# Kernel tuning notes

Hardware: AMD Instinct MI355X
Metric: run time of the kernel (lower is better)

Reference implementation:

```python
import jax, jax.numpy as jnp
import numpy as np
import math

B, S, D, H = 2, 2048, 1024, 16
DK = D // H


def setup_inputs() -> dict:
    key = jax.random.key(0)
    ks = jax.random.split(key, 10)
    sc = 1.0 / math.sqrt(D)
    inp = {
        "Q_input": jax.random.normal(ks[0], (B, S, D), dtype=jnp.float32),
        "Wq_w": jax.random.normal(ks[1], (D, D), dtype=jnp.float32) * sc,
        "Wq_b": jnp.zeros((D,), dtype=jnp.float32),
        "Wk_w": jax.random.normal(ks[2], (D, D), dtype=jnp.float32) * sc,
        "Wk_b": jnp.zeros((D,), dtype=jnp.float32),
        "Wv_w": jax.random.normal(ks[3], (D, D), dtype=jnp.float32) * sc,
        "Wv_b": jnp.zeros((D,), dtype=jnp.float32),
        "Wo_w": jax.random.normal(ks[4], (D, D), dtype=jnp.float32) * sc,
        "Wo_b": jnp.zeros((D,), dtype=jnp.float32),
        # causal mask, broadcast over batch and heads: [1,1,S,S]
        "mask": jnp.tril(jnp.ones((S, S), dtype=jnp.int32))[None, None],
    }
    return inp


def reference(Q_input, Wq_w, Wq_b, Wk_w, Wk_b, Wv_w, Wv_b, Wo_w, Wo_b, mask):
    b, s, _ = Q_input.shape
    # linear projections (torch Linear: x @ W^T + b)
    Q = Q_input @ Wq_w.T + Wq_b
    K = Q_input @ Wk_w.T + Wk_b
    V = Q_input @ Wv_w.T + Wv_b
    # [b, h, s, dk]
    Q = Q.reshape(b, s, H, DK).transpose(0, 2, 1, 3)
    K = K.reshape(b, s, H, DK).transpose(0, 2, 1, 3)
    V = V.reshape(b, s, H, DK).transpose(0, 2, 1, 3)
    scores = jnp.einsum("bhqd,bhkd->bhqk", Q, K) / math.sqrt(DK)
    scores = jnp.where(mask == 0, jnp.float32(-1e9), scores)
    weights = jax.nn.softmax(scores, axis=-1)
    attn = jnp.einsum("bhqk,bhkd->bhqd", weights, V)
    attn = attn.transpose(0, 2, 1, 3).reshape(b, s, D)
    return attn @ Wo_w.T + Wo_b
```

## Files before the change

### kernel.cpp

```cpp
#include <hip/hip_runtime.h>
#include <hip/hip_bf16.h>
#include <cstdint>

typedef __attribute__((ext_vector_type(8))) short short8;
typedef __attribute__((ext_vector_type(4))) float f32x4;
typedef __attribute__((ext_vector_type(2))) unsigned int uint2v;
typedef unsigned short ushort_t;

#define S_LEN 2048
#define D_DIM 1024
#define NH 16
#define DK 64
#define BATCH 2
#define M_ROWS (BATCH * S_LEN)
#define BK 32

__device__ inline ushort_t f2bf(float f) {
    union { float f; uint32_t u; } v; v.f = f;
    uint32_t r = v.u + 0x7fffu + ((v.u >> 16) & 1u);
    return (ushort_t)(r >> 16);
}

__device__ __forceinline__ ushort_t bfc(float f) {
    __hip_bfloat16 h = __float2bfloat16(f);
    return __builtin_bit_cast(ushort_t, h);
}

__device__ __forceinline__ float bf2f(ushort_t u) {
    return __uint_as_float(((uint32_t)u) << 16);
}

__device__ __forceinline__ float fexp2(float x) {
#if __has_builtin(__builtin_amdgcn_exp2f)
    return __builtin_amdgcn_exp2f(x);
#else
    return exp2f(x);
#endif
}
__device__ __forceinline__ float frcp(float x) {
#if __has_builtin(__builtin_amdgcn_rcpf)
    return __builtin_amdgcn_rcpf(x);
#else
    return 1.0f / x;
#endif
}

__device__ __forceinline__ void glds16(const ushort_t* g, ushort_t* l) {
    __builtin_amdgcn_global_load_lds(
        (const __attribute__((address_space(1))) uint32_t*)g,
        (__attribute__((address_space(3))) uint32_t*)l,
        16, 0, 0);
}

#if __has_builtin(__builtin_amdgcn_permlane16_swap) && __has_builtin(__builtin_amdgcn_permlane32_swap)
#define HAS_PLSWAP 1
#else
#define HAS_PLSWAP 0
#endif

__device__ __forceinline__ float red_max4(float x) {
#if HAS_PLSWAP
    uint2v a = __builtin_amdgcn_permlane16_swap(__float_as_uint(x), __float_as_uint(x), false, false);
    float y = fmaxf(__uint_as_float(a.x), __uint_as_float(a.y));
    uint2v b = __builtin_amdgcn_permlane32_swap(__float_as_uint(y), __float_as_uint(y), false, false);
    return fmaxf(__uint_as_float(b.x), __uint_as_float(b.y));
#else
    x = fmaxf(x, __shfl_xor(x, 16));
    return fmaxf(x, __shfl_xor(x, 32));
#endif
}
__device__ __forceinline__ float red_sum4(float x) {
#if HAS_PLSWAP
    uint2v a = __builtin_amdgcn_permlane16_swap(__float_as_uint(x), __float_as_uint(x), false, false);
    float y = __uint_as_float(a.x) + __uint_as_float(a.y);
    uint2v b = __builtin_amdgcn_permlane32_swap(__float_as_uint(y), __float_as_uint(y), false, false);
    return __uint_as_float(b.x) + __uint_as_float(b.y);
#else
    x += __shfl_xor(x, 16);
    return x + __shfl_xor(x, 32);
#endif
}

__device__ __forceinline__ void route_p(const uint32_t wp[4][2], int ks, int lane, uint32_t F[4]) {
#if HAS_PLSWAP
    uint32_t U0 = wp[2 * ks][0],     U1 = wp[2 * ks][1];
    uint32_t V0 = wp[2 * ks + 1][0], V1 = wp[2 * ks + 1][1];
    uint2v t, pa0, pa1, pb0, pb1;
    t = __builtin_amdgcn_permlane32_swap(U0, U0, false, false);
    pa0 = __builtin_amdgcn_permlane16_swap(U0, t.y, false, false);
    t = __builtin_amdgcn_permlane32_swap(U1, U1, false, false);
    pa1 = __builtin_amdgcn_permlane16_swap(U1, t.y, false, false);
    t = __builtin_amdgcn_permlane32_swap(V0, V0, false, false);
    pb0 = __builtin_amdgcn_permlane16_swap(t.x, V0, false, false);
    t = __builtin_amdgcn_permlane32_swap(V1, V1, false, false);
    pb1 = __builtin_amdgcn_permlane16_swap(t.x, V1, false, false);
    bool lo = lane < 32;
    F[0] = lo ? pa0.x : pb0.x;
    F[1] = lo ? pa1.x : pb1.x;
    F[2] = lo ? pa0.y : pb0.y;
    F[3] = lo ? pa1.y : pb1.y;
#else
    int q = lane & 15, g = lane >> 4;
#pragma unroll
    for (int m = 0; m < 4; m++) {
        int src = 16 * (2 * (g & 1) + (m >> 1)) + q;
        uint32_t xa = (uint32_t)__shfl((int)wp[2 * ks][m & 1], src);
        uint32_t xb = (uint32_t)__shfl((int)wp[2 * ks + 1][m & 1], src);
        F[m] = (g < 2) ? xa : xb;
    }
#endif
}

__global__ void cvt_bf16(const float* __restrict__ in, ushort_t* __restrict__ out, int n4) {
    int i = blockIdx.x * blockDim.x + threadIdx.x;
    int stride = gridDim.x * blockDim.x;
    for (int idx = i; idx < n4; idx += stride) {
        float4 v = ((const float4*)in)[idx];
        ushort4 o;
        o.x = f2bf(v.x); o.y = f2bf(v.y); o.z = f2bf(v.z); o.w = f2bf(v.w);
        ((ushort4*)out)[idx] = o;
    }
}

__global__ void cvt_w3(const float* __restrict__ wq, const float* __restrict__ wk,
                       const float* __restrict__ wv, ushort_t* __restrict__ wqkv) {
    const int seg = (D_DIM * D_DIM) / 4;
    int i = blockIdx.x * blockDim.x + threadIdx.x;
    int stride = gridDim.x * blockDim.x;
    for (int idx = i; idx < 3 * seg; idx += stride) {
        int sel = idx >> 18;
        int id = idx & (seg - 1);
        const float* src = sel == 0 ? wq : (sel == 1 ? wk : wv);
        float4 v = ((const float4*)src)[id];
        ushort4 o;
        o.x = f2bf(v.x); o.y = f2bf(v.y); o.z = f2bf(v.z); o.w = f2bf(v.w);
        ((ushort4*)wqkv)[sel * seg + id] = o;
    }
}

template<int MODE, int BMt, int BNt>
__global__ __launch_bounds__(256, 3) void gemm_bt(const ushort_t* __restrict__ A,
                                                  const ushort_t* __restrict__ Bw,
                                                  const float* __restrict__ b0,
                                                  const float* __restrict__ b1,
                                                  const float* __restrict__ b2,
                                                  void* __restrict__ C0,
                                                  void* __restrict__ C1,
                                                  void* __restrict__ C2,
                                                  int M, int N, int K) {
    constexpr int FM = BMt / 32, FN = BNt / 32;
    constexpr int ACH = BMt / 64, BCH = BNt / 64;
    __shared__ ushort_t As[2][BMt * BK];
    __shared__ ushort_t Bs[2][BNt * BK];
    int tid = threadIdx.x;
    int lane = tid & 63;
    int w = tid >> 6;
    int wr = w >> 1, wc = w & 1;
    int nwg = gridDim.x;
    int bx = (blockIdx.x & 7) * (nwg >> 3) + (blockIdx.x >> 3);
    int ntile = N / BNt;
    int m0 = (bx / ntile) * BMt;
    int n0 = (bx % ntile) * BNt;
    int lr = lane & 15;
    int lk = (lane >> 4) * 8;
    int srow = lane >> 2;
    int scol = (lane & 3) * 8;

    auto stage = [&](int b, int kt) {
#pragma unroll
        for (int c = 0; c < ACH; c++)
            glds16(&A[(size_t)(m0 + w * (BMt / 4) + c * 16 + srow) * K + kt + scol],
                   &As[b][(w * (BMt / 4) + c * 16) * BK]);
#pragma unroll
        for (int c = 0; c < BCH; c++)
            glds16(&Bw[(size_t)(n0 + w * (BNt / 4) + c * 16 + srow) * K + kt + scol],
                   &Bs[b][(w * (BNt / 4) + c * 16) * BK]);
    };

    f32x4 acc[FM][FN] = {};

    stage(0, 0);
    __syncthreads();
    int cur = 0;
    for (int kt = 0; kt < K; kt += BK) {
        if (kt + BK < K) stage(cur ^ 1, kt + BK);

        short8 af[FM], bf[FN];
#pragma unroll
        for (int f = 0; f < FM; f++)
            af[f] = *(const short8*)&As[cur][(wr * (BMt / 2) + f * 16 + lr) * BK + lk];
#pragma unroll
        for (int f = 0; f < FN; f++)
            bf[f] = *(const short8*)&Bs[cur][(wc * (BNt / 2) + f * 16 + lr) * BK + lk];
#pragma unroll
        for (int i = 0; i < FM; i++)
#pragma unroll
            for (int j = 0; j < FN; j++)
                acc[i][j] = __builtin_amdgcn_mfma_f32_16x16x32_bf16(af[i], bf[j], acc[i][j], 0, 0, 0);

        __syncthreads();
        cur ^= 1;
    }

    int r0 = (lane >> 4) * 4;
#pragma unroll
    for (int j = 0; j < FN; j++) {
        int ncol = n0 + wc * (BNt / 2) + j * 16 + lr;
        if (MODE == 2) {
            float bv = b0[ncol];
#pragma unroll
            for (int i = 0; i < FM; i++) {
                int mbase = m0 + wr * (BMt / 2) + i * 16 + r0;
#pragma unroll
                for (int r = 0; r < 4; r++)
                    ((float*)C0)[(size_t)(mbase + r) * N + ncol] = acc[i][j][r] + bv;
            }
        } else {
            int sel = n0 >> 10;
            const float* bp = sel == 0 ? b0 : (sel == 1 ? b1 : b2);
            int nc = ncol & 1023;
            float bv = bp[nc];
            int hh = nc >> 6, dk = nc & 63;
            ushort_t* Co = (ushort_t*)(sel == 0 ? C0 : (sel == 1 ? C1 : C2));
#pragma unroll
            for (int i = 0; i < FM; i++) {
                int mbase = m0 + wr * (BMt / 2) + i * 16 + r0;
                int bb = mbase >> 11, ss = mbase & 2047;
                if (sel == 2) {
                    ushort4 pk;
                    pk.x = f2bf(acc[i][j][0] + bv);
                    pk.y = f2bf(acc[i][j][1] + bv);
                    pk.z = f2bf(acc[i][j][2] + bv);
                    pk.w = f2bf(acc[i][j][3] + bv);
                    size_t idx = ((size_t)(bb * NH + hh) * DK + dk) * S_LEN + ss;
                    *(ushort4*)&Co[idx] = pk;
                } else {
#pragma unroll
                    for (int r = 0; r < 4; r++) {
                        size_t idx = ((size_t)(bb * NH + hh) * S_LEN + (ss + r)) * DK + dk;
                        Co[idx] = f2bf(acc[i][j][r] + bv);
                    }
                }
            }
        }
    }
}

#define CSC 0.1803368801f

__device__ const unsigned char JTAB[40] = {
    23,22,21,20,19,18,17,16,
    31,31,30,28,29,26,27,15,
    24,25,30,28,29,27,26,14,
    24,11, 9,10, 8,25,12,13,
     0, 1, 2, 4, 6, 5, 7, 3};
__device__ const unsigned char KTAB[40] = {
     9, 9, 9, 9, 9, 9, 9, 9,
     0, 1, 0, 0, 0, 0, 1, 9,
     0, 0, 1, 1, 1, 0, 1, 9,
     1, 9, 9, 9, 9, 1, 9, 9,
     9, 9, 9, 9, 9, 9, 9, 9};

__global__ __launch_bounds__(256, 5) void attn_fwd(const ushort_t* __restrict__ Q,
                                                   const ushort_t* __restrict__ K,
                                                   const ushort_t* __restrict__ Vt,
                                                   ushort_t* __restrict__ Oa,
                                                   float2* __restrict__ ml,
                                                   float* __restrict__ Pd) {
    __shared__ ushort_t Ks[2][64 * 64];
    __shared__ ushort_t Vs[2][64 * 64];

    int tid = threadIdx.x;
    int lane = tid & 63;
    int w = tid >> 6;
    int bh = blockIdx.x;
    int yy = blockIdx.y;
    int j = JTAB[yy];
    int kk = KTAB[yy];
    int nt = j + 1;
    int half = (nt + 1) >> 1;
    int t0 = (kk == 1) ? half : 0;
    int t1 = (kk == 0) ? half : nt;
    int cnt = t1 - t0;
    int off = yy % cnt;
    size_t base = (size_t)bh * S_LEN * DK;
    int q0 = j * 64;

    int lr = lane & 15;
    int lk = (lane >> 4) * 8;
    int g16 = (lane >> 4) * 16;
    int r0 = (lane >> 4) * 4;
    int wq = w * 16 + lr;

    int swb = (lr & 7) << 4;
    int swLo = (lr * 128 + (g16 ^ swb)) >> 1;
    int swHi = (lr * 128 + ((64 + g16) ^ swb)) >> 1;

    short8 qf0 = *(const short8*)&Q[base + (size_t)(q0 + wq) * DK + lk];
    short8 qf1 = *(const short8*)&Q[base + (size_t)(q0 + wq) * DK + 32 + lk];

    f32x4 o[4] = {};
    float mrowL = -1e30f, lrow = 0.f;

    int sr = tid >> 3;
    int scb = (tid & 7) * 16;
    int wOff = (sr * 128 + (scb ^ ((sr & 7) << 4))) >> 1;

    const ushort_t* kBase = K  + base + (size_t)sr * DK + ((tid & 7) * 8);
    const ushort_t* vBase = Vt + base + (size_t)sr * S_LEN + ((tid & 7) * 8);

    int tf = t0 + off;
    {
        const ushort_t* kp = kBase + (size_t)tf * (64 * DK);
        const ushort_t* vp = vBase + (size_t)tf * 64;
        *(uint4*)&Ks[0][wOff]        = *(const uint4*)kp;
        *(uint4*)&Ks[0][wOff + 2048] = *(const uint4*)(kp + 32 * DK);
        *(uint4*)&Vs[0][wOff]        = *(const uint4*)vp;
        *(uint4*)&Vs[0][wOff + 2048] = *(const uint4*)(vp + 32 * S_LEN);
    }
    __syncthreads();

    int t = tf;
    int tpre = (tf == t1 - 1) ? t0 : tf + 1;
    const ushort_t* kPre = kBase + (size_t)tpre * (64 * DK);
    const ushort_t* vPre = vBase + (size_t)tpre * 64;

    int cur = 0;
    for (int s = 0; s < cnt; ++s) {
        bool last = (s == cnt - 1);
        bool diag = (t == j);
        uint4 kr0, kr1, vr0, vr1;
        if (!last) {
            kr0 = *(const uint4*)kPre;
            kr1 = *(const uint4*)(kPre + 32 * DK);
            vr0 = *(const uint4*)vPre;
            vr1 = *(const uint4*)(vPre + 32 * S_LEN);
        }

        f32x4 st[4] = {};
        __builtin_amdgcn_s_setprio(1);
#pragma unroll
        for (int n = 0; n < 4; n++) {
            if (!diag || n <= w) {
                short8 kf0 = *(const short8*)&Ks[cur][swLo + n * 1024];
                short8 kf1 = *(const short8*)&Ks[cur][swHi + n * 1024];
                st[n] = __builtin_amdgcn_mfma_f32_16x16x32_bf16(kf0, qf0, st[n], 0, 0, 0);
                st[n] = __builtin_amdgcn_mfma_f32_16x16x32_bf16(kf1, qf1, st[n], 0, 0, 0);
            }
        }
        __builtin_amdgcn_s_setprio(0);

        if (diag) {
#pragma unroll
            for (int n = 0; n < 4; n++)
#pragma unroll
                for (int i = 0; i < 4; i++)
                    if (16 * n + r0 + i > wq) st[n][i] = -1e30f;
        }

        float m0 = fmaxf(fmaxf(fmaxf(st[0][0], st[0][1]), st[0][2]), st[0][3]);
        float m1 = fmaxf(fmaxf(fmaxf(st[1][0], st[1][1]), st[1][2]), st[1][3]);
        float m2 = fmaxf(fmaxf(fmaxf(st[2][0], st[2][1]), st[2][2]), st[2][3]);
        float m3 = fmaxf(fmaxf(fmaxf(st[3][0], st[3][1]), st[3][2]), st[3][3]);
        float mx = fmaxf(fmaxf(fmaxf(m0, m1), m2), m3);
        float mxL = red_max4(mx) * CSC;

        bool skip = __all(mxL <= mrowL + 8.0f);
        float corr = 1.0f;
        float mnewL = mrowL;
        if (!skip) {
            mnewL = fmaxf(mrowL, mxL);
            corr = fexp2(mrowL - mnewL);
            mrowL = mnewL;
        }

        float psum = 0.f;
        uint32_t wp[4][2];
#pragma unroll
        for (int n = 0; n < 4; n++) {
#pragma unroll
            for (int i = 0; i < 4; i++) {
                float p = fexp2(fmaf(st[n][i], CSC, -mnewL));
                st[n][i] = p;
                psum += p;
            }
            wp[n][0] = (uint32_t)bfc(st[n][0]) | ((uint32_t)bfc(st[n][1]) << 16);
            wp[n][1] = (uint32_t)bfc(st[n][2]) | ((uint32_t)bfc(st[n][3]) << 16);
        }
        psum = red_sum4(psum);

        if (skip) {
            lrow += psum;
        } else {
            lrow = lrow * corr + psum;
            float cb[4];
#pragma unroll
            for (int i = 0; i < 4; i++) cb[i] = __shfl(corr, r0 + i);
#pragma unroll
            for (int d = 0; d < 4; d++)
#pragma unroll
                for (int i = 0; i < 4; i++) o[d][i] *= cb[i];
        }

#pragma unroll
        for (int ks = 0; ks < 2; ks++) {
            if (diag && 32 * ks > w * 16 + 15) continue;
            uint32_t F[4];
            route_p(wp, ks, lane, F);
            union { uint32_t u[4]; short8 s; } pu;
            pu.u[0] = F[0]; pu.u[1] = F[1]; pu.u[2] = F[2]; pu.u[3] = F[3];
            short8 pf = pu.s;
            int vb = (ks ? swHi : swLo);
            __builtin_amdgcn_s_setprio(1);
#pragma unroll
            for (int d = 0; d < 4; d++) {
                short8 vf = *(const short8*)&Vs[cur][vb + d * 1024];
                o[d] = __builtin_amdgcn_mfma_f32_16x16x32_bf16(pf, vf, o[d], 0, 0, 0);
            }
            __builtin_amdgcn_s_setprio(0);
        }

        if (!last) {
            *(uint4*)&Ks[cur ^ 1][wOff]        = kr0;
            *(uint4*)&Ks[cur ^ 1][wOff + 2048] = kr1;
            *(uint4*)&Vs[cur ^ 1][wOff]        = vr0;
            *(uint4*)&Vs[cur ^ 1][wOff + 2048] = vr1;
        }
        __syncthreads();
        cur ^= 1;

        t = tpre;
        bool wrap = (tpre == t1 - 1);
        tpre = wrap ? t0 : tpre + 1;
        kPre += wrap ? -(ptrdiff_t)(cnt - 1) * (64 * DK) : (ptrdiff_t)(64 * DK);
        vPre += wrap ? -(ptrdiff_t)(cnt - 1) * 64 : (ptrdiff_t)64;
    }

    int b = bh >> 4, h = bh & 15;
    if (kk == 9) {
        float lb[4];
#pragma unroll
        for (int i = 0; i < 4; i++) lb[i] = frcp(__shfl(lrow, r0 + i));
#pragma unroll
        for (int d = 0; d < 4; d++)
#pragma unroll
            for (int i = 0; i < 4; i++) {
                int qq = q0 + w * 16 + r0 + i;
                int dk = d * 16 + lr;
                size_t idx = ((size_t)(b * S_LEN + qq)) * D_DIM + h * DK + dk;
                Oa[idx] = bfc(o[d][i] * lb[i]);
            }
    } else {
        int jj = j - 24;
        if (kk == 0) {
#pragma unroll
            for (int d = 0; d < 4; d++)
#pragma unroll
                for (int i = 0; i < 4; i++) {
                    int qq = q0 + w * 16 + r0 + i;
                    int dk = d * 16 + lr;
                    size_t idx = ((size_t)(b * S_LEN + qq)) * D_DIM + h * DK + dk;
                    Oa[idx] = bfc(o[d][i]);
                }
        } else {
#pragma unroll
            for (int d = 0; d < 4; d++)
#pragma unroll
                for (int i = 0; i < 4; i++) {
                    int rloc = w * 16 + r0 + i;
                    Pd[((size_t)(bh * 8 + jj) * 64 + rloc) * 64 + d * 16 + lr] = o[d][i];
                }
        }
        if (lane < 16) {
            int row = w * 16 + lane;
            ml[(size_t)kk * 16384 + (bh * 8 + jj) * 64 + row] = make_float2(mrowL, lrow);
        }
    }
}

__global__ __launch_bounds__(256) void attn_merge(const float2* __restrict__ ml,
                                                  const float* __restrict__ Pd,
                                                  ushort_t* __restrict__ Oa) {
    int bh = blockIdx.x;
    int jj = blockIdx.y;
    int tid = threadIdx.x;
    int r = tid >> 2;
    int q = (tid & 3) * 16;
    int b = bh >> 4, h = bh & 15;
    int row = (jj + 24) * 64 + r;
    float2 a = ml[(bh * 8 + jj) * 64 + r];
    float2 c = ml[16384 + (bh * 8 + jj) * 64 + r];
    float M = fmaxf(a.x, c.x);
    float w0 = fexp2(a.x - M), w1 = fexp2(c.x - M);
    float rc = frcp(a.y * w0 + c.y * w1);
    size_t ob = ((size_t)(b * S_LEN + row)) * D_DIM + h * DK + q;
    const float* p1 = &Pd[((size_t)(bh * 8 + jj) * 64 + r) * 64 + q];
#pragma unroll
    for (int i = 0; i < 4; i++) {
        ushort4 o0 = *(const ushort4*)&Oa[ob + i * 4];
        float4 o1 = *(const float4*)&p1[i * 4];
        ushort4 res;
        res.x = bfc((bf2f(o0.x) * w0 + o1.x * w1) * rc);
        res.y = bfc((bf2f(o0.y) * w0 + o1.y * w1) * rc);
        res.z = bfc((bf2f(o0.z) * w0 + o1.z * w1) * rc);
        res.w = bfc((bf2f(o0.w) * w0 + o1.w * w1) * rc);
        *(ushort4*)&Oa[ob + i * 4] = res;
    }
}

extern "C" void kernel_launch(void* const* d_in, const int* in_sizes, int n_in,
                              void* d_out, int out_size, void* d_ws, size_t ws_size,
                              hipStream_t stream) {
    const float* X  = (const float*)d_in[0];
    const float* Wq = (const float*)d_in[1];
    const float* bq = (const float*)d_in[2];
    const float* Wk = (const float*)d_in[3];
    const float* bk = (const float*)d_in[4];
    const float* Wv = (const float*)d_in[5];
    const float* bv = (const float*)d_in[6];
    const float* Wo = (const float*)d_in[7];
    const float* bo = (const float*)d_in[8];
    float* out = (float*)d_out;

    char* ws = (char*)d_ws;
    ushort_t* Xb    = (ushort_t*)ws;
    ushort_t* Wqkvb = (ushort_t*)(ws + (8u  << 20));
    float2*   mlbuf = (float2*)(ws + (8u  << 20));
    ushort_t* Qb    = (ushort_t*)(ws + (14u << 20));
    ushort_t* Kb    = (ushort_t*)(ws + (22u << 20));
    ushort_t* Vtb   = (ushort_t*)(ws + (30u << 20));
    ushort_t* Wob   = Wqkvb;
    ushort_t* Ab    = Xb;
    float*    Pd    = out;

    const int M = M_ROWS;
    int nX4 = (M * D_DIM) / 4;
    int nW4 = (D_DIM * D_DIM) / 4;

    cvt_bf16<<<2048, 256, 0, stream>>>(X, Xb, nX4);
    cvt_w3<<<2048, 256, 0, stream>>>(Wq, Wk, Wv, Wqkvb);

    gemm_bt<3, 128, 128><<<dim3((M / 128) * (3072 / 128)), 256, 0, stream>>>(
        Xb, Wqkvb, bq, bk, bv, Qb, Kb, Vtb, M, 3072, D_DIM);

    dim3 agrid(BATCH * NH, 40);
    attn_fwd<<<agrid, 256, 0, stream>>>(Qb, Kb, Vtb, Ab, mlbuf, Pd);

    attn_merge<<<dim3(BATCH * NH, 8), 256, 0, stream>>>(mlbuf, Pd, Ab);

    cvt_bf16<<<2048, 256, 0, stream>>>(Wo, Wob, nW4);

    gemm_bt<2, 64, 128><<<dim3((M / 64) * (D_DIM / 128)), 256, 0, stream>>>(
        Ab, Wob, bo, bo, bo, out, out, out, M, D_DIM, D_DIM);
}
```

Measured before the change: 118.8 us.

## Rebalance causal attention work split and vectorize GEMM epilogue stores

Replaces the attention block schedule table so that 14 query tiles per head, instead of 8, are split in two halves, and lets some blocks process two short query tiles in sequence. The merge kernel is widened to match. The aim is a more even amount of work per block across the 40-block grid. Separately, the GEMM swaps the MFMA operand order for the Q/K and output projections so each lane holds four consecutive columns, which allows vectorized float4/ushort4 epilogue stores and bias loads. The trade-off is more partial-result traffic through Pd and ml, and extra merge work.

```diff
diff --git a/kernel.cpp b/kernel.cpp
--- a/kernel.cpp
+++ b/kernel.cpp
@@ -14,6 +14,8 @@
 #define BATCH 2
 #define M_ROWS (BATCH * S_LEN)
 #define BK 32
+#define NSPL 14
+#define MLSTR (32 * NSPL * 64)
 
 __device__ inline ushort_t f2bf(float f) {
     union { float f; uint32_t u; } v; v.f = f;
@@ -165,6 +167,8 @@
     int lk = (lane >> 4) * 8;
     int srow = lane >> 2;
     int scol = (lane & 3) * 8;
+    int sel = n0 >> 10;
+    bool swp = (MODE == 2) || (sel < 2);
 
     auto stage = [&](int b, int kt) {
 #pragma unroll
@@ -192,55 +196,82 @@
 #pragma unroll
         for (int f = 0; f < FN; f++)
             bf[f] = *(const short8*)&Bs[cur][(wc * (BNt / 2) + f * 16 + lr) * BK + lk];
-#pragma unroll
-        for (int i = 0; i < FM; i++)
-#pragma unroll
-            for (int j = 0; j < FN; j++)
-                acc[i][j] = __builtin_amdgcn_mfma_f32_16x16x32_bf16(af[i], bf[j], acc[i][j], 0, 0, 0);
+        if (swp) {
+#pragma unroll
+            for (int i = 0; i < FM; i++)
+#pragma unroll
+                for (int j = 0; j < FN; j++)
+                    acc[i][j] = __builtin_amdgcn_mfma_f32_16x16x32_bf16(bf[j], af[i], acc[i][j], 0, 0, 0);
+        } else {
+#pragma unroll
+            for (int i = 0; i < FM; i++)
+#pragma unroll
+                for (int j = 0; j < FN; j++)
+                    acc[i][j] = __builtin_amdgcn_mfma_f32_16x16x32_bf16(af[i], bf[j], acc[i][j], 0, 0, 0);
+        }
 
         __syncthreads();
         cur ^= 1;
     }
 
     int r0 = (lane >> 4) * 4;
-#pragma unroll
-    for (int j = 0; j < FN; j++) {
-        int ncol = n0 + wc * (BNt / 2) + j * 16 + lr;
-        if (MODE == 2) {
-            float bv = b0[ncol];
+    if (MODE == 2) {
+#pragma unroll
+        for (int j = 0; j < FN; j++) {
+            int nc0 = n0 + wc * (BNt / 2) + j * 16 + r0;
+            float4 bv = *(const float4*)&b0[nc0];
 #pragma unroll
             for (int i = 0; i < FM; i++) {
-                int mbase = m0 + wr * (BMt / 2) + i * 16 + r0;
-#pragma unroll
-                for (int r = 0; r < 4; r++)
-                    ((float*)C0)[(size_t)(mbase + r) * N + ncol] = acc[i][j][r] + bv;
-            }
-        } else {
-            int sel = n0 >> 10;
-            const float* bp = sel == 0 ? b0 : (sel == 1 ? b1 : b2);
+                int mm = m0 + wr * (BMt / 2) + i * 16 + lr;
+                float4 v;
+                v.x = acc[i][j][0] + bv.x;
+                v.y = acc[i][j][1] + bv.y;
+                v.z = acc[i][j][2] + bv.z;
+                v.w = acc[i][j][3] + bv.w;
+                *(float4*)&((float*)C0)[(size_t)mm * N + nc0] = v;
+            }
+        }
+    } else if (sel < 2) {
+        ushort_t* Co = (ushort_t*)(sel == 0 ? C0 : C1);
+        const float* bp = sel == 0 ? b0 : b1;
+#pragma unroll
+        for (int j = 0; j < FN; j++) {
+            int nc0 = (n0 + wc * (BNt / 2) + j * 16 + r0) & 1023;
+            int hh = nc0 >> 6, dk0 = nc0 & 63;
+            float4 bv = *(const float4*)&bp[nc0];
+#pragma unroll
+            for (int i = 0; i < FM; i++) {
+                int mm = m0 + wr * (BMt / 2) + i * 16 + lr;
+                int bb = mm >> 11, ss = mm & 2047;
+                ushort4 pk;
+                pk.x = f2bf(acc[i][j][0] + bv.x);
+                pk.y = f2bf(acc[i][j][1] + bv.y);
+                pk.z = f2bf(acc[i][j][2] + bv.z);
+                pk.w = f2bf(acc[i][j][3] + bv.w);
+                size_t idx = ((size_t)(bb * NH + hh) * S_LEN + ss) * DK + dk0;
+                *(ushort4*)&Co[idx] = pk;
+            }
+        }
+    } else {
+        ushort_t* Co = (ushort_t*)C2;
+        const float* bp = b2;
+#pragma unroll
+        for (int j = 0; j < FN; j++) {
+            int ncol = n0 + wc * (BNt / 2) + j * 16 + lr;
             int nc = ncol & 1023;
             float bv = bp[nc];
             int hh = nc >> 6, dk = nc & 63;
-            ushort_t* Co = (ushort_t*)(sel == 0 ? C0 : (sel == 1 ? C1 : C2));
 #pragma unroll
             for (int i = 0; i < FM; i++) {
                 int mbase = m0 + wr * (BMt / 2) + i * 16 + r0;
                 int bb = mbase >> 11, ss = mbase & 2047;
-                if (sel == 2) {
-                    ushort4 pk;
-                    pk.x = f2bf(acc[i][j][0] + bv);
-                    pk.y = f2bf(acc[i][j][1] + bv);
-                    pk.z = f2bf(acc[i][j][2] + bv);
-                    pk.w = f2bf(acc[i][j][3] + bv);
-                    size_t idx = ((size_t)(bb * NH + hh) * DK + dk) * S_LEN + ss;
-                    *(ushort4*)&Co[idx] = pk;
-                } else {
-#pragma unroll
-                    for (int r = 0; r < 4; r++) {
-                        size_t idx = ((size_t)(bb * NH + hh) * S_LEN + (ss + r)) * DK + dk;
-                        Co[idx] = f2bf(acc[i][j][r] + bv);
-                    }
-                }
+                ushort4 pk;
+                pk.x = f2bf(acc[i][j][0] + bv);
+                pk.y = f2bf(acc[i][j][1] + bv);
+                pk.z = f2bf(acc[i][j][2] + bv);
+                pk.w = f2bf(acc[i][j][3] + bv);
+                size_t idx = ((size_t)(bb * NH + hh) * DK + dk) * S_LEN + ss;
+                *(ushort4*)&Co[idx] = pk;
             }
         }
     }
@@ -249,17 +280,17 @@
 #define CSC 0.1803368801f
 
 __device__ const unsigned char JTAB[40] = {
-    23,22,21,20,19,18,17,16,
-    31,31,30,28,29,26,27,15,
-    24,25,30,28,29,27,26,14,
-    24,11, 9,10, 8,25,12,13,
-     0, 1, 2, 4, 6, 5, 7, 3};
+    17,16,15,30,31,31,13,27,
+    24,18,18,19,19,20,26,28,
+    12,14,28,29,29,30,27,25,
+    11,10, 9, 8, 7,25,23,26,
+     6,20,21,21,22,22,23,24};
 __device__ const unsigned char KTAB[40] = {
-     9, 9, 9, 9, 9, 9, 9, 9,
-     0, 1, 0, 0, 0, 0, 1, 9,
-     0, 0, 1, 1, 1, 0, 1, 9,
-     1, 9, 9, 9, 9, 1, 9, 9,
-     9, 9, 9, 9, 9, 9, 9, 9};
+     9, 9, 9, 0, 0, 1, 9, 1,
+     0, 1, 0, 0, 1, 1, 0, 1,
+    10, 9, 0, 0, 1, 1, 0, 1,
+    11,12,13,14,15, 0, 0, 1,
+     9, 0, 0, 1, 1, 0, 1, 1};
 
 __global__ __launch_bounds__(256, 5) void attn_fwd(const ushort_t* __restrict__ Q,
                                                    const ushort_t* __restrict__ K,
@@ -275,16 +306,10 @@
     int w = tid >> 6;
     int bh = blockIdx.x;
     int yy = blockIdx.y;
-    int j = JTAB[yy];
-    int kk = KTAB[yy];
-    int nt = j + 1;
-    int half = (nt + 1) >> 1;
-    int t0 = (kk == 1) ? half : 0;
-    int t1 = (kk == 0) ? half : nt;
-    int cnt = t1 - t0;
-    int off = yy % cnt;
+    int JT = JTAB[yy];
+    int KT = KTAB[yy];
+    int nseg = (KT >= 10) ? 2 : 1;
     size_t base = (size_t)bh * S_LEN * DK;
-    int q0 = j * 64;
 
     int lr = lane & 15;
     int lk = (lane >> 4) * 8;
@@ -296,163 +321,162 @@
     int swLo = (lr * 128 + (g16 ^ swb)) >> 1;
     int swHi = (lr * 128 + ((64 + g16) ^ swb)) >> 1;
 
-    short8 qf0 = *(const short8*)&Q[base + (size_t)(q0 + wq) * DK + lk];
-    short8 qf1 = *(const short8*)&Q[base + (size_t)(q0 + wq) * DK + 32 + lk];
-
-    f32x4 o[4] = {};
-    float mrowL = -1e30f, lrow = 0.f;
-
     int sr = tid >> 3;
     int scb = (tid & 7) * 16;
     int wOff = (sr * 128 + (scb ^ ((sr & 7) << 4))) >> 1;
 
     const ushort_t* kBase = K  + base + (size_t)sr * DK + ((tid & 7) * 8);
     const ushort_t* vBase = Vt + base + (size_t)sr * S_LEN + ((tid & 7) * 8);
-
-    int tf = t0 + off;
-    {
-        const ushort_t* kp = kBase + (size_t)tf * (64 * DK);
-        const ushort_t* vp = vBase + (size_t)tf * 64;
-        *(uint4*)&Ks[0][wOff]        = *(const uint4*)kp;
-        *(uint4*)&Ks[0][wOff + 2048] = *(const uint4*)(kp + 32 * DK);
-        *(uint4*)&Vs[0][wOff]        = *(const uint4*)vp;
-        *(uint4*)&Vs[0][wOff + 2048] = *(const uint4*)(vp + 32 * S_LEN);
-    }
-    __syncthreads();
-
-    int t = tf;
-    int tpre = (tf == t1 - 1) ? t0 : tf + 1;
-    const ushort_t* kPre = kBase + (size_t)tpre * (64 * DK);
-    const ushort_t* vPre = vBase + (size_t)tpre * 64;
-
-    int cur = 0;
-    for (int s = 0; s < cnt; ++s) {
-        bool last = (s == cnt - 1);
-        bool diag = (t == j);
-        uint4 kr0, kr1, vr0, vr1;
-        if (!last) {
-            kr0 = *(const uint4*)kPre;
-            kr1 = *(const uint4*)(kPre + 32 * DK);
-            vr0 = *(const uint4*)vPre;
-            vr1 = *(const uint4*)(vPre + 32 * S_LEN);
-        }
-
-        f32x4 st[4] = {};
-        __builtin_amdgcn_s_setprio(1);
-#pragma unroll
-        for (int n = 0; n < 4; n++) {
-            if (!diag || n <= w) {
-                short8 kf0 = *(const short8*)&Ks[cur][swLo + n * 1024];
-                short8 kf1 = *(const short8*)&Ks[cur][swHi + n * 1024];
-                st[n] = __builtin_amdgcn_mfma_f32_16x16x32_bf16(kf0, qf0, st[n], 0, 0, 0);
-                st[n] = __builtin_amdgcn_mfma_f32_16x16x32_bf16(kf1, qf1, st[n], 0, 0, 0);
-            }
-        }
-        __builtin_amdgcn_s_setprio(0);
-
-        if (diag) {
-#pragma unroll
-            for (int n = 0; n < 4; n++)
-#pragma unroll
-                for (int i = 0; i < 4; i++)
-                    if (16 * n + r0 + i > wq) st[n][i] = -1e30f;
-        }
-
-        float m0 = fmaxf(fmaxf(fmaxf(st[0][0], st[0][1]), st[0][2]), st[0][3]);
-        float m1 = fmaxf(fmaxf(fmaxf(st[1][0], st[1][1]), st[1][2]), st[1][3]);
-        float m2 = fmaxf(fmaxf(fmaxf(st[2][0], st[2][1]), st[2][2]), st[2][3]);
-        float m3 = fmaxf(fmaxf(fmaxf(st[3][0], st[3][1]), st[3][2]), st[3][3]);
-        float mx = fmaxf(fmaxf(fmaxf(m0, m1), m2), m3);
-        float mxL = red_max4(mx) * CSC;
-
-        bool skip = __all(mxL <= mrowL + 8.0f);
-        float corr = 1.0f;
-        float mnewL = mrowL;
-        if (!skip) {
-            mnewL = fmaxf(mrowL, mxL);
-            corr = fexp2(mrowL - mnewL);
-            mrowL = mnewL;
-        }
-
-        float psum = 0.f;
-        uint32_t wp[4][2];
-#pragma unroll
-        for (int n = 0; n < 4; n++) {
-#pragma unroll
-            for (int i = 0; i < 4; i++) {
-                float p = fexp2(fmaf(st[n][i], CSC, -mnewL));
-                st[n][i] = p;
-                psum += p;
-            }
-            wp[n][0] = (uint32_t)bfc(st[n][0]) | ((uint32_t)bfc(st[n][1]) << 16);
-            wp[n][1] = (uint32_t)bfc(st[n][2]) | ((uint32_t)bfc(st[n][3]) << 16);
-        }
-        psum = red_sum4(psum);
-
-        if (skip) {
-            lrow += psum;
-        } else {
-            lrow = lrow * corr + psum;
-            float cb[4];
-#pragma unroll
-            for (int i = 0; i < 4; i++) cb[i] = __shfl(corr, r0 + i);
-#pragma unroll
-            for (int d = 0; d < 4; d++)
-#pragma unroll
-                for (int i = 0; i < 4; i++) o[d][i] *= cb[i];
-        }
-
-#pragma unroll
-        for (int ks = 0; ks < 2; ks++) {
-            if (diag && 32 * ks > w * 16 + 15) continue;
-            uint32_t F[4];
-            route_p(wp, ks, lane, F);
-            union { uint32_t u[4]; short8 s; } pu;
-            pu.u[0] = F[0]; pu.u[1] = F[1]; pu.u[2] = F[2]; pu.u[3] = F[3];
-            short8 pf = pu.s;
-            int vb = (ks ? swHi : swLo);
+    int b = bh >> 4, h = bh & 15;
+
+    for (int seg = 0; seg < nseg; ++seg) {
+        int j = (seg == 0) ? JT : (KT - 10);
+        int kk = (KT <= 1) ? KT : 9;
+        int nt = j + 1;
+        int half = (nt + 1) >> 1;
+        int t0 = (kk == 1) ? half : 0;
+        int t1 = (kk == 0) ? half : nt;
+        int cnt = t1 - t0;
+        int off = yy % cnt;
+        int q0 = j * 64;
+
+        short8 qf0 = *(const short8*)&Q[base + (size_t)(q0 + wq) * DK + lk];
+        short8 qf1 = *(const short8*)&Q[base + (size_t)(q0 + wq) * DK + 32 + lk];
+
+        f32x4 o[4] = {};
+        float mrowL = -1e30f, lrow = 0.f;
+
+        int tf = t0 + off;
+        {
+            const ushort_t* kp = kBase + (size_t)tf * (64 * DK);
+            const ushort_t* vp = vBase + (size_t)tf * 64;
+            *(uint4*)&Ks[0][wOff]        = *(const uint4*)kp;
+            *(uint4*)&Ks[0][wOff + 2048] = *(const uint4*)(kp + 32 * DK);
+            *(uint4*)&Vs[0][wOff]        = *(const uint4*)vp;
+            *(uint4*)&Vs[0][wOff + 2048] = *(const uint4*)(vp + 32 * S_LEN);
+        }
+        __syncthreads();
+
+        int t = tf;
+        int tpre = (tf == t1 - 1) ? t0 : tf + 1;
+        const ushort_t* kPre = kBase + (size_t)tpre * (64 * DK);
+        const ushort_t* vPre = vBase + (size_t)tpre * 64;
+
+        int cur = 0;
+        for (int s = 0; s < cnt; ++s) {
+            bool last = (s == cnt - 1);
+            bool diag = (t == j);
+            uint4 kr0, kr1, vr0, vr1;
+            if (!last) {
+                kr0 = *(const uint4*)kPre;
+                kr1 = *(const uint4*)(kPre + 32 * DK);
+                vr0 = *(const uint4*)vPre;
+                vr1 = *(const uint4*)(vPre + 32 * S_LEN);
+            }
+
+            f32x4 st[4] = {};
             __builtin_amdgcn_s_setprio(1);
 #pragma unroll
-            for (int d = 0; d < 4; d++) {
-                short8 vf = *(const short8*)&Vs[cur][vb + d * 1024];
-                o[d] = __builtin_amdgcn_mfma_f32_16x16x32_bf16(pf, vf, o[d], 0, 0, 0);
+            for (int n = 0; n < 4; n++) {
+                if (!diag || n <= w) {
+                    short8 kf0 = *(const short8*)&Ks[cur][swLo + n * 1024];
+                    short8 kf1 = *(const short8*)&Ks[cur][swHi + n * 1024];
+                    st[n] = __builtin_amdgcn_mfma_f32_16x16x32_bf16(kf0, qf0, st[n], 0, 0, 0);
+                    st[n] = __builtin_amdgcn_mfma_f32_16x16x32_bf16(kf1, qf1, st[n], 0, 0, 0);
+                }
             }
             __builtin_amdgcn_s_setprio(0);
-        }
-
-        if (!last) {
-            *(uint4*)&Ks[cur ^ 1][wOff]        = kr0;
-            *(uint4*)&Ks[cur ^ 1][wOff + 2048] = kr1;
-            *(uint4*)&Vs[cur ^ 1][wOff]        = vr0;
-            *(uint4*)&Vs[cur ^ 1][wOff + 2048] = vr1;
-        }
-        __syncthreads();
-        cur ^= 1;
-
-        t = tpre;
-        bool wrap = (tpre == t1 - 1);
-        tpre = wrap ? t0 : tpre + 1;
-        kPre += wrap ? -(ptrdiff_t)(cnt - 1) * (64 * DK) : (ptrdiff_t)(64 * DK);
-        vPre += wrap ? -(ptrdiff_t)(cnt - 1) * 64 : (ptrdiff_t)64;
-    }
-
-    int b = bh >> 4, h = bh & 15;
-    if (kk == 9) {
-        float lb[4];
-#pragma unroll
-        for (int i = 0; i < 4; i++) lb[i] = frcp(__shfl(lrow, r0 + i));
-#pragma unroll
-        for (int d = 0; d < 4; d++)
-#pragma unroll
-            for (int i = 0; i < 4; i++) {
-                int qq = q0 + w * 16 + r0 + i;
-                int dk = d * 16 + lr;
-                size_t idx = ((size_t)(b * S_LEN + qq)) * D_DIM + h * DK + dk;
-                Oa[idx] = bfc(o[d][i] * lb[i]);
-            }
-    } else {
-        int jj = j - 24;
-        if (kk == 0) {
+
+            if (diag) {
+#pragma unroll
+                for (int n = 0; n < 4; n++)
+#pragma unroll
+                    for (int i = 0; i < 4; i++)
+                        if (16 * n + r0 + i > wq) st[n][i] = -1e30f;
+            }
+
+            float m0 = fmaxf(fmaxf(fmaxf(st[0][0], st[0][1]), st[0][2]), st[0][3]);
+            float m1 = fmaxf(fmaxf(fmaxf(st[1][0], st[1][1]), st[1][2]), st[1][3]);
+            float m2 = fmaxf(fmaxf(fmaxf(st[2][0], st[2][1]), st[2][2]), st[2][3]);
+            float m3 = fmaxf(fmaxf(fmaxf(st[3][0], st[3][1]), st[3][2]), st[3][3]);
+            float mx = fmaxf(fmaxf(fmaxf(m0, m1), m2), m3);
+            float mxL = red_max4(mx) * CSC;
+
+            bool skip = __all(mxL <= mrowL + 8.0f);
+            float corr = 1.0f;
+            float mnewL = mrowL;
+            if (!skip) {
+                mnewL = fmaxf(mrowL, mxL);
+                corr = fexp2(mrowL - mnewL);
+                mrowL = mnewL;
+            }
+
+            float psum = 0.f;
+            uint32_t wp[4][2];
+#pragma unroll
+            for (int n = 0; n < 4; n++) {
+#pragma unroll
+                for (int i = 0; i < 4; i++) {
+                    float p = fexp2(fmaf(st[n][i], CSC, -mnewL));
+                    st[n][i] = p;
+                    psum += p;
+                }
+                wp[n][0] = (uint32_t)bfc(st[n][0]) | ((uint32_t)bfc(st[n][1]) << 16);
+                wp[n][1] = (uint32_t)bfc(st[n][2]) | ((uint32_t)bfc(st[n][3]) << 16);
+            }
+            psum = red_sum4(psum);
+
+            if (skip) {
+                lrow += psum;
+            } else {
+                lrow = lrow * corr + psum;
+                float cb[4];
+#pragma unroll
+                for (int i = 0; i < 4; i++) cb[i] = __shfl(corr, r0 + i);
+#pragma unroll
+                for (int d = 0; d < 4; d++)
+#pragma unroll
+                    for (int i = 0; i < 4; i++) o[d][i] *= cb[i];
+            }
+
+#pragma unroll
+            for (int ks = 0; ks < 2; ks++) {
+                if (diag && 32 * ks > w * 16 + 15) continue;
+                uint32_t F[4];
+                route_p(wp, ks, lane, F);
+                union { uint32_t u[4]; short8 s; } pu;
+                pu.u[0] = F[0]; pu.u[1] = F[1]; pu.u[2] = F[2]; pu.u[3] = F[3];
+                short8 pf = pu.s;
+                int vb = (ks ? swHi : swLo);
+                __builtin_amdgcn_s_setprio(1);
+#pragma unroll
+                for (int d = 0; d < 4; d++) {
+                    short8 vf = *(const short8*)&Vs[cur][vb + d * 1024];
+                    o[d] = __builtin_amdgcn_mfma_f32_16x16x32_bf16(pf, vf, o[d], 0, 0, 0);
+                }
+                __builtin_amdgcn_s_setprio(0);
+            }
+
+            if (!last) {
+                *(uint4*)&Ks[cur ^ 1][wOff]        = kr0;
+                *(uint4*)&Ks[cur ^ 1][wOff + 2048] = kr1;
+                *(uint4*)&Vs[cur ^ 1][wOff]        = vr0;
+                *(uint4*)&Vs[cur ^ 1][wOff + 2048] = vr1;
+            }
+            __syncthreads();
+            cur ^= 1;
+
+            t = tpre;
+            bool wrap = (tpre == t1 - 1);
+            tpre = wrap ? t0 : tpre + 1;
+            kPre += wrap ? -(ptrdiff_t)(cnt - 1) * (64 * DK) : (ptrdiff_t)(64 * DK);
+            vPre += wrap ? -(ptrdiff_t)(cnt - 1) * 64 : (ptrdiff_t)64;
+        }
+
+        if (kk == 9) {
+            float lb[4];
+#pragma unroll
+            for (int i = 0; i < 4; i++) lb[i] = frcp(__shfl(lrow, r0 + i));
 #pragma unroll
             for (int d = 0; d < 4; d++)
 #pragma unroll
@@ -460,20 +484,33 @@
                     int qq = q0 + w * 16 + r0 + i;
                     int dk = d * 16 + lr;
                     size_t idx = ((size_t)(b * S_LEN + qq)) * D_DIM + h * DK + dk;
-                    Oa[idx] = bfc(o[d][i]);
+                    Oa[idx] = bfc(o[d][i] * lb[i]);
                 }
         } else {
-#pragma unroll
-            for (int d = 0; d < 4; d++)
-#pragma unroll
-                for (int i = 0; i < 4; i++) {
-                    int rloc = w * 16 + r0 + i;
-                    Pd[((size_t)(bh * 8 + jj) * 64 + rloc) * 64 + d * 16 + lr] = o[d][i];
-                }
-        }
-        if (lane < 16) {
-            int row = w * 16 + lane;
-            ml[(size_t)kk * 16384 + (bh * 8 + jj) * 64 + row] = make_float2(mrowL, lrow);
+            int jj = j - 18;
+            if (kk == 0) {
+#pragma unroll
+                for (int d = 0; d < 4; d++)
+#pragma unroll
+                    for (int i = 0; i < 4; i++) {
+                        int qq = q0 + w * 16 + r0 + i;
+                        int dk = d * 16 + lr;
+                        size_t idx = ((size_t)(b * S_LEN + qq)) * D_DIM + h * DK + dk;
+                        Oa[idx] = bfc(o[d][i]);
+                    }
+            } else {
+#pragma unroll
+                for (int d = 0; d < 4; d++)
+#pragma unroll
+                    for (int i = 0; i < 4; i++) {
+                        int rloc = w * 16 + r0 + i;
+                        Pd[((size_t)(bh * NSPL + jj) * 64 + rloc) * 64 + d * 16 + lr] = o[d][i];
+                    }
+            }
+            if (lane < 16) {
+                int row = w * 16 + lane;
+                ml[(size_t)kk * MLSTR + (bh * NSPL + jj) * 64 + row] = make_float2(mrowL, lrow);
+            }
         }
     }
 }
@@ -487,14 +524,14 @@
     int r = tid >> 2;
     int q = (tid & 3) * 16;
     int b = bh >> 4, h = bh & 15;
-    int row = (jj + 24) * 64 + r;
-    float2 a = ml[(bh * 8 + jj) * 64 + r];
-    float2 c = ml[16384 + (bh * 8 + jj) * 64 + r];
+    int row = (jj + 18) * 64 + r;
+    float2 a = ml[(bh * NSPL + jj) * 64 + r];
+    float2 c = ml[MLSTR + (bh * NSPL + jj) * 64 + r];
     float M = fmaxf(a.x, c.x);
     float w0 = fexp2(a.x - M), w1 = fexp2(c.x - M);
     float rc = frcp(a.y * w0 + c.y * w1);
     size_t ob = ((size_t)(b * S_LEN + row)) * D_DIM + h * DK + q;
-    const float* p1 = &Pd[((size_t)(bh * 8 + jj) * 64 + r) * 64 + q];
+    const float* p1 = &Pd[((size_t)(bh * NSPL + jj) * 64 + r) * 64 + q];
 #pragma unroll
     for (int i = 0; i < 4; i++) {
         ushort4 o0 = *(const ushort4*)&Oa[ob + i * 4];
@@ -546,7 +583,7 @@
     dim3 agrid(BATCH * NH, 40);
     attn_fwd<<<agrid, 256, 0, stream>>>(Qb, Kb, Vtb, Ab, mlbuf, Pd);
 
-    attn_merge<<<dim3(BATCH * NH, 8), 256, 0, stream>>>(mlbuf, Pd, Ab);
+    attn_merge<<<dim3(BATCH * NH, NSPL), 256, 0, stream>>>(mlbuf, Pd, Ab);
 
     cvt_bf16<<<2048, 256, 0, stream>>>(Wo, Wob, nW4);
 
```

Result: slower. 153.9 us (+29.5%).
